# Performance work log

Hardware: AMD Instinct MI355X
Metric: run time of the kernel (lower is better)

Reference implementation:

```python
import jax, jax.numpy as jnp
import numpy as np

B, R, L, V, D, P, K = 512, 20, 50, 50000, 64, 2, 10
IN_DIM = 2 * P * D
TAU = 0.5


def _gating(x, w1, w2, b2, bg):
    # sigmoid(xW1^T) + bg * tanh(xW2^T + b2)
    return jax.nn.sigmoid(x @ w1.T) + bg * jnp.tanh(x @ w2.T + b2)


def _coatt_scores(u, i, w, b, M):
    uo = jax.nn.relu(u @ w.T + b)
    io = jax.nn.relu(i @ w.T + b)
    # bilinear scores: U @ M @ I^T
    return jnp.einsum('bud,de,bve->buv', uo, M, io)


def _gumbel_hard(logits, key):
    g = jax.random.gumbel(key, logits.shape, logits.dtype)
    y = jax.nn.softmax((logits + g) / TAU, axis=-1)
    yh = jax.nn.one_hot(jnp.argmax(y, axis=-1), logits.shape[-1], dtype=y.dtype)
    return y + jax.lax.stop_gradient(yh - y)  # straight-through hard one-hot


def _forward(user_reviews, item_reviews, emb, gate_w1, gate_w2, gate_b2, gate_bg,
             ra_w, ra_b, ra_M, wa_w, wa_b, wa_M, fm_v, fm_w, fm_b):
    u_emb = emb[user_reviews]            # [B,R,L,D]
    i_emb = emb[item_reviews]            # [B,R,L,D]
    u_rev = _gating(u_emb.sum(axis=-2), gate_w1, gate_w2, gate_b2, gate_bg)  # [B,R,D]
    i_rev = _gating(i_emb.sum(axis=-2), gate_w1, gate_w2, gate_b2, gate_bg)  # [B,R,D]
    key = jax.random.key(42)
    u_reprs, i_reprs = [], []
    for p in range(P):
        s = _coatt_scores(u_rev, i_rev, ra_w, ra_b, ra_M)     # [B,R,R]
        pr = _gumbel_hard(s.max(axis=-1), jax.random.fold_in(key, 2 * p))
        pc = _gumbel_hard(s.max(axis=-2), jax.random.fold_in(key, 2 * p + 1))
        # hard one-hot pointer 'gather' expressed as weighted sum over review axis
        ur = jnp.einsum('br,brld->bld', pr, u_emb)            # [B,L,D]
        ir = jnp.einsum('br,brld->bld', pc, i_emb)            # [B,L,D]
        sw = _coatt_scores(ur, ir, wa_w, wa_b, wa_M)          # [B,L,L]
        wr = jax.nn.softmax(sw.mean(axis=-1), axis=-1)        # [B,L]
        wc = jax.nn.softmax(sw.mean(axis=-2), axis=-1)        # [B,L]
        u_reprs.append(jnp.einsum('bl,bld->bd', wr, ur))
        i_reprs.append(jnp.einsum('bl,bld->bd', wc, ir))
    x = jnp.concatenate(u_reprs + i_reprs, axis=-1)           # [B, 2*P*D]
    lin = x @ fm_w.T + fm_b                                   # [B,1]
    i1 = x @ fm_v
    i2 = (x * x) @ (fm_v * fm_v)
    pair = jnp.sum(i1 * i1 - i2, axis=-1)                     # [B]
    return (lin[:, 0] + 0.5 * pair)[:, None]                  # [B,1]


def setup_inputs() -> dict:
    key = jax.random.key(0)
    ks = jax.random.split(key, 20)
    return {
        'user_reviews': jax.random.randint(ks[0], (B, R, L), 0, V, dtype=jnp.int32),
        'item_reviews': jax.random.randint(ks[1], (B, R, L), 0, V, dtype=jnp.int32),
        'emb': jax.random.normal(ks[2], (V, D), jnp.float32) * 0.1,
        'gate_w1': jax.random.normal(ks[3], (D, D), jnp.float32) * 0.05,
        'gate_w2': jax.random.normal(ks[4], (D, D), jnp.float32) * 0.05,
        'gate_b2': jax.random.normal(ks[5], (D,), jnp.float32) * 0.05,
        'gate_bg': jax.random.normal(ks[6], (D,), jnp.float32) * 0.05,
        'ra_w': jax.random.normal(ks[7], (D, D), jnp.float32) * 0.05,
        'ra_b': jax.random.normal(ks[8], (D,), jnp.float32) * 0.05,
        'ra_M': jax.random.normal(ks[9], (D, D), jnp.float32) * 0.05,
        'wa_w': jax.random.normal(ks[10], (D, D), jnp.float32) * 0.05,
        'wa_b': jax.random.normal(ks[11], (D,), jnp.float32) * 0.05,
        'wa_M': jax.random.normal(ks[12], (D, D), jnp.float32) * 0.05,
        'fm_v': jax.random.normal(ks[13], (IN_DIM, K), jnp.float32) * 0.05,
        'fm_w': jax.random.normal(ks[14], (1, IN_DIM), jnp.float32) * 0.05,
        'fm_b': jax.random.normal(ks[15], (1,), jnp.float32) * 0.05,
    }


def reference(user_reviews, item_reviews, emb, gate_w1, gate_w2, gate_b2, gate_bg,
              ra_w, ra_b, ra_M, wa_w, wa_b, wa_M, fm_v, fm_w, fm_b):
    return _forward(user_reviews, item_reviews, emb, gate_w1, gate_w2, gate_b2, gate_bg,
                    ra_w, ra_b, ra_M, wa_w, wa_b, wa_M, fm_v, fm_w, fm_b)
```

## Files before the change

kernel.cpp:

```cpp
#include <hip/hip_runtime.h>
#include <stdint.h>
#include <math.h>

#define BB 512
#define RR 20
#define LL 50
#define DD 64
#define PP 2
#define KK 10
#define IN_DIM 256
#define VV 50000
#define NEBLK 1280
#define NTBLK 782

__device__ __forceinline__ uint32_t rotl32(uint32_t v, int d) {
  return (v << d) | (v >> (32 - d));
}

__device__ __forceinline__ void tf2x32(uint32_t k0, uint32_t k1,
                                       uint32_t x0, uint32_t x1,
                                       uint32_t& o0, uint32_t& o1) {
  uint32_t ks0 = k0, ks1 = k1, ks2 = k0 ^ k1 ^ 0x1BD11BDAu;
  x0 += ks0; x1 += ks1;
#define TF_RND(r) { x0 += x1; x1 = rotl32(x1, r); x1 ^= x0; }
  TF_RND(13) TF_RND(15) TF_RND(26) TF_RND(6)
  x0 += ks1; x1 += ks2 + 1u;
  TF_RND(17) TF_RND(29) TF_RND(16) TF_RND(24)
  x0 += ks2; x1 += ks0 + 2u;
  TF_RND(13) TF_RND(15) TF_RND(26) TF_RND(6)
  x0 += ks0; x1 += ks1 + 3u;
  TF_RND(17) TF_RND(29) TF_RND(16) TF_RND(24)
  x0 += ks1; x1 += ks2 + 4u;
  TF_RND(13) TF_RND(15) TF_RND(26) TF_RND(6)
  x0 += ks2; x1 += ks0 + 5u;
#undef TF_RND
  o0 = x0; o1 = x1;
}

__device__ __forceinline__ float wave_sum(float v) {
  for (int off = 32; off; off >>= 1) v += __shfl_xor(v, off, 64);
  return v;
}
__device__ __forceinline__ float wave_max(float v) {
  for (int off = 32; off; off >>= 1) v = fmaxf(v, __shfl_xor(v, off, 64));
  return v;
}

__global__ __launch_bounds__(256) void transpose_w(
    const float* __restrict__ w1, const float* __restrict__ w2,
    const float* __restrict__ ra, const float* __restrict__ wa,
    const float* __restrict__ ma,
    float* __restrict__ w1T, float* __restrict__ w2T,
    float* __restrict__ raT, float* __restrict__ waT,
    float* __restrict__ maT) {
  int i = blockIdx.x * 256 + threadIdx.x;
  if (i < DD * DD) {
    int r = i >> 6, c = i & 63;
    w1T[c * DD + r] = w1[i];
    w2T[c * DD + r] = w2[i];
    raT[c * DD + r] = ra[i];
    waT[c * DD + r] = wa[i];
    maT[c * DD + r] = ma[i];
  }
}

__global__ __launch_bounds__(256, 4) void tables_embed(
    const int* __restrict__ uidx, const int* __restrict__ iidx,
    const float* __restrict__ emb,
    const float* __restrict__ w1T, const float* __restrict__ w2T,
    const float* __restrict__ b2, const float* __restrict__ bg,
    const float* __restrict__ waT, const float* __restrict__ wa_b,
    const float* __restrict__ maT,
    float* __restrict__ u_rev, float* __restrict__ i_rev,
    float* __restrict__ E1, float* __restrict__ E2) {
  __shared__ float smemA[DD * 68];
  __shared__ float smemB[DD * 68];
  int tid = threadIdx.x;
  int bid = blockIdx.x;

  if (bid < NEBLK) {
    int* idxs = (int*)smemA;
    float (*us)[68] = (float(*)[68])(smemA + 800);
    int isItem = (bid >= 640);
    const int* src = isItem ? (iidx + (size_t)(bid - 640) * 16 * LL)
                            : (uidx + (size_t)bid * 16 * LL);
    for (int i = tid; i < 16 * LL; i += 256) idxs[i] = src[i];
    __syncthreads();
    int w = tid >> 6, lane = tid & 63;
    int grp = lane >> 4, q = lane & 15;
    int revl = w * 4 + grp;
    const int* myidx = idxs + revl * LL;
    float4 acc = {0.f, 0.f, 0.f, 0.f};
#pragma unroll
    for (int l = 0; l < LL; ++l) {
      int v = myidx[l];
      float4 e4 = *reinterpret_cast<const float4*>(&emb[(size_t)v * DD + q * 4]);
      acc.x += e4.x; acc.y += e4.y; acc.z += e4.z; acc.w += e4.w;
    }
    *reinterpret_cast<float4*>(&us[revl][q * 4]) = acc;
    __syncthreads();
    float4 d1 = {0.f, 0.f, 0.f, 0.f}, d2 = {0.f, 0.f, 0.f, 0.f};
    for (int e = 0; e < DD; ++e) {
      float xv = us[revl][e];
      float4 w1v = *reinterpret_cast<const float4*>(&w1T[e * DD + q * 4]);
      float4 w2v = *reinterpret_cast<const float4*>(&w2T[e * DD + q * 4]);
      d1.x += xv * w1v.x; d1.y += xv * w1v.y; d1.z += xv * w1v.z; d1.w += xv * w1v.w;
      d2.x += xv * w2v.x; d2.y += xv * w2v.y; d2.z += xv * w2v.z; d2.w += xv * w2v.w;
    }
    float4 b2v = *reinterpret_cast<const float4*>(&b2[q * 4]);
    float4 bgv = *reinterpret_cast<const float4*>(&bg[q * 4]);
    float4 val;
    val.x = 1.f / (1.f + expf(-d1.x)) + bgv.x * tanhf(d2.x + b2v.x);
    val.y = 1.f / (1.f + expf(-d1.y)) + bgv.y * tanhf(d2.y + b2v.y);
    val.z = 1.f / (1.f + expf(-d1.z)) + bgv.z * tanhf(d2.z + b2v.z);
    val.w = 1.f / (1.f + expf(-d1.w)) + bgv.w * tanhf(d2.w + b2v.w);
    int gid = bid * 16 + revl;
    int t = gid - isItem * (BB * RR);
    float* dst = isItem ? i_rev : u_rev;
    *reinterpret_cast<float4*>(&dst[(size_t)t * DD + q * 4]) = val;
    return;
  }

  float* A  = smemA;
  float* Bs = smemB;
  int v0 = (bid - NEBLK) * 64;
  {
    int wr = tid & 63;
    int qk = tid >> 6;
    int v = v0 + wr;
    for (int rep = 0; rep < 4; ++rep) {
      int k0 = rep * 16 + qk * 4;
      float4 e4 = {0.f, 0.f, 0.f, 0.f};
      if (v < VV) e4 = *reinterpret_cast<const float4*>(&emb[(size_t)v * DD + k0]);
      A[(k0 + 0) * 68 + wr] = e4.x;
      A[(k0 + 1) * 68 + wr] = e4.y;
      A[(k0 + 2) * 68 + wr] = e4.z;
      A[(k0 + 3) * 68 + wr] = e4.w;
    }
  }
  for (int i = tid; i < DD * 16; i += 256) {
    int k = i >> 4, c = i & 15;
    *reinterpret_cast<float4*>(&Bs[k * 68 + c * 4]) =
        *reinterpret_cast<const float4*>(&waT[k * DD + c * 4]);
  }
  __syncthreads();
  int wq = tid & 15, dq = tid >> 4;
  float4 bias = *reinterpret_cast<const float4*>(&wa_b[dq * 4]);
  float acc[4][4];
#pragma unroll
  for (int i = 0; i < 4; ++i) {
    acc[i][0] = bias.x; acc[i][1] = bias.y; acc[i][2] = bias.z; acc[i][3] = bias.w;
  }
  for (int k = 0; k < DD; ++k) {
    float4 a4 = *reinterpret_cast<const float4*>(&A[k * 68 + wq * 4]);
    float4 b4 = *reinterpret_cast<const float4*>(&Bs[k * 68 + dq * 4]);
    float av[4] = {a4.x, a4.y, a4.z, a4.w};
    float bv[4] = {b4.x, b4.y, b4.z, b4.w};
#pragma unroll
    for (int i = 0; i < 4; ++i)
#pragma unroll
      for (int j = 0; j < 4; ++j) acc[i][j] += av[i] * bv[j];
  }
#pragma unroll
  for (int i = 0; i < 4; ++i)
#pragma unroll
    for (int j = 0; j < 4; ++j) acc[i][j] = fmaxf(acc[i][j], 0.f);
#pragma unroll
  for (int i = 0; i < 4; ++i) {
    int v = v0 + wq * 4 + i;
    if (v < VV) {
      float4 r = {acc[i][0], acc[i][1], acc[i][2], acc[i][3]};
      *reinterpret_cast<float4*>(&E1[(size_t)v * DD + dq * 4]) = r;
    }
  }
  __syncthreads();
#pragma unroll
  for (int j = 0; j < 4; ++j)
#pragma unroll
    for (int i = 0; i < 4; ++i)
      A[(dq * 4 + j) * 68 + wq * 4 + i] = acc[i][j];
  for (int i = tid; i < DD * 16; i += 256) {
    int k = i >> 4, c = i & 15;
    *reinterpret_cast<float4*>(&Bs[k * 68 + c * 4]) =
        *reinterpret_cast<const float4*>(&maT[k * DD + c * 4]);
  }
  __syncthreads();
  float acc2[4][4];
#pragma unroll
  for (int i = 0; i < 4; ++i)
#pragma unroll
    for (int j = 0; j < 4; ++j) acc2[i][j] = 0.f;
  for (int k = 0; k < DD; ++k) {
    float4 a4 = *reinterpret_cast<const float4*>(&A[k * 68 + wq * 4]);
    float4 b4 = *reinterpret_cast<const float4*>(&Bs[k * 68 + dq * 4]);
    float av[4] = {a4.x, a4.y, a4.z, a4.w};
    float bv[4] = {b4.x, b4.y, b4.z, b4.w};
#pragma unroll
    for (int i = 0; i < 4; ++i)
#pragma unroll
      for (int j = 0; j < 4; ++j) acc2[i][j] += av[i] * bv[j];
  }
#pragma unroll
  for (int i = 0; i < 4; ++i) {
    int v = v0 + wq * 4 + i;
    if (v < VV) {
      float4 r = {acc2[i][0], acc2[i][1], acc2[i][2], acc2[i][3]};
      *reinterpret_cast<float4*>(&E2[(size_t)v * DD + dq * 4]) = r;
    }
  }
}

__global__ __launch_bounds__(256) void coatt_rev_sel(
    const float* __restrict__ u_rev, const float* __restrict__ i_rev,
    const float* __restrict__ raT, const float* __restrict__ ra_b,
    const float* __restrict__ ra_M, int* __restrict__ sel) {
  int b = blockIdx.x;
  __shared__ float ur[RR * 68], ir[RR * 68], uo[RR * 68], io[RR * 68], au[RR * 68];
  __shared__ float sc[RR * 21];
  __shared__ float rl[RR], cl[RR];
  __shared__ float gval[4][RR];
  int tid = threadIdx.x;
  for (int i = tid; i < RR * 16; i += 256) {
    int r = i >> 4, qq = i & 15;
    *reinterpret_cast<float4*>(&ur[r * 68 + qq * 4]) =
        *reinterpret_cast<const float4*>(&u_rev[(size_t)b * RR * DD + r * DD + qq * 4]);
    *reinterpret_cast<float4*>(&ir[r * 68 + qq * 4]) =
        *reinterpret_cast<const float4*>(&i_rev[(size_t)b * RR * DD + r * DD + qq * 4]);
  }
  __syncthreads();
  for (int s = tid; s < RR * 16; s += 256) {
    int u = s >> 4, q = s & 15;
    float4 bias = *reinterpret_cast<const float4*>(&ra_b[q * 4]);
    float4 a1 = bias, a2 = bias;
    for (int e = 0; e < DD; ++e) {
      float xu = ur[u * 68 + e];
      float xi = ir[u * 68 + e];
      float4 wv = *reinterpret_cast<const float4*>(&raT[e * DD + q * 4]);
      a1.x += xu * wv.x; a1.y += xu * wv.y; a1.z += xu * wv.z; a1.w += xu * wv.w;
      a2.x += xi * wv.x; a2.y += xi * wv.y; a2.z += xi * wv.z; a2.w += xi * wv.w;
    }
    a1.x = fmaxf(a1.x, 0.f); a1.y = fmaxf(a1.y, 0.f);
    a1.z = fmaxf(a1.z, 0.f); a1.w = fmaxf(a1.w, 0.f);
    a2.x = fmaxf(a2.x, 0.f); a2.y = fmaxf(a2.y, 0.f);
    a2.z = fmaxf(a2.z, 0.f); a2.w = fmaxf(a2.w, 0.f);
    *reinterpret_cast<float4*>(&uo[u * 68 + q * 4]) = a1;
    *reinterpret_cast<float4*>(&io[u * 68 + q * 4]) = a2;
  }
  __syncthreads();
  for (int s = tid; s < RR * 16; s += 256) {
    int u = s >> 4, q = s & 15;
    float4 a = {0.f, 0.f, 0.f, 0.f};
    for (int d2 = 0; d2 < DD; ++d2) {
      float xv = uo[u * 68 + d2];
      float4 mv = *reinterpret_cast<const float4*>(&ra_M[d2 * DD + q * 4]);
      a.x += xv * mv.x; a.y += xv * mv.y; a.z += xv * mv.z; a.w += xv * mv.w;
    }
    *reinterpret_cast<float4*>(&au[u * 68 + q * 4]) = a;
  }
  __syncthreads();
  for (int i = tid; i < RR * RR; i += 256) {
    int u = i / RR, v = i % RR;
    float a = 0.f;
    for (int e = 0; e < DD; ++e) a += au[u * 68 + e] * io[v * 68 + e];
    sc[u * 21 + v] = a;
  }
  __syncthreads();
  if (tid < RR) {
    float m = -INFINITY;
    for (int v = 0; v < RR; ++v) m = fmaxf(m, sc[tid * 21 + v]);
    rl[tid] = m;
  } else if (tid >= 64 && tid < 64 + RR) {
    int v = tid - 64;
    float m = -INFINITY;
    for (int u = 0; u < RR; ++u) m = fmaxf(m, sc[u * 21 + v]);
    cl[v] = m;
  }
  __syncthreads();
  if (tid < 4 * RR) {
    int n = tid / RR, r = tid % RR;
    uint32_t k0, k1, o0, o1;
    tf2x32(0u, 42u, 0u, (uint32_t)n, k0, k1);
    int e = b * RR + r;
    tf2x32(k0, k1, 0u, (uint32_t)e, o0, o1);
    uint32_t bits = o0 ^ o1;
    float u01 = __uint_as_float((bits >> 9) | 0x3f800000u) - 1.0f;
    const float TINY = 1.1754943508222875e-38f;
    float u = fmaxf(u01 + TINY, TINY);
    float g = -logf(-logf(u));
    gval[n][r] = ((n & 1) ? cl[r] : rl[r]) + g;
  }
  __syncthreads();
  if (tid < 4) {
    float best = -INFINITY; int arg = 0;
    for (int r = 0; r < RR; ++r) {
      float v = gval[tid][r];
      if (v > best) { best = v; arg = r; }
    }
    sel[tid * BB + b] = arg;
  }
}

__global__ __launch_bounds__(256) void word_coatt(
    const int* __restrict__ uidx, const int* __restrict__ iidx,
    const float* __restrict__ emb,
    const float* __restrict__ E1, const float* __restrict__ E2,
    const int* __restrict__ sel, float* __restrict__ x) {
  int bid = blockIdx.x;
  int p = bid >> 9, b = bid & (BB - 1);
  int ru = sel[(2 * p) * BB + b];
  int rv = sel[(2 * p + 1) * BB + b];
  __shared__ int uw[LL], iw[LL];
  __shared__ float E1u[LL * 65], E2i[LL * 65];
  __shared__ float ubar[DD], zbar[DD];
  __shared__ float rm[LL], cm[LL];
  int tid = threadIdx.x;
  if (tid < LL) uw[tid] = uidx[((size_t)b * RR + ru) * LL + tid];
  else if (tid >= 64 && tid < 64 + LL) iw[tid - 64] = iidx[((size_t)b * RR + rv) * LL + (tid - 64)];
  __syncthreads();
  for (int i = tid; i < LL * DD; i += 256) {
    int l = i >> 6, d = i & 63;
    E1u[l * 65 + d] = E1[(size_t)uw[l] * DD + d];
    E2i[l * 65 + d] = E2[(size_t)iw[l] * DD + d];
  }
  __syncthreads();
  if (tid < DD) {
    float s = 0.f;
    for (int l = 0; l < LL; ++l) s += E1u[l * 65 + tid];
    ubar[tid] = s / 50.f;
  } else if (tid < 128) {
    int d = tid - 64;
    float s = 0.f;
    for (int l = 0; l < LL; ++l) s += E2i[l * 65 + d];
    zbar[d] = s / 50.f;
  }
  __syncthreads();
  if (tid < LL) {
    float a = 0.f;
    for (int e = 0; e < DD; ++e) a += E1u[tid * 65 + e] * zbar[e];
    rm[tid] = a;
  } else if (tid >= 64 && tid < 64 + LL) {
    int lj = tid - 64;
    float a = 0.f;
    for (int e = 0; e < DD; ++e) a += ubar[e] * E2i[lj * 65 + e];
    cm[lj] = a;
  }
  __syncthreads();
  int w = tid >> 6, lane = tid & 63;
  if (w == 0) {
    float v = (lane < LL) ? rm[lane] : -INFINITY;
    float m = wave_max(v);
    float ex = (lane < LL) ? expf(rm[lane] - m) : 0.f;
    float sm = wave_sum(ex);
    if (lane < LL) rm[lane] = ex / sm;
  } else if (w == 1) {
    float v = (lane < LL) ? cm[lane] : -INFINITY;
    float m = wave_max(v);
    float ex = (lane < LL) ? expf(cm[lane] - m) : 0.f;
    float sm = wave_sum(ex);
    if (lane < LL) cm[lane] = ex / sm;
  }
  __syncthreads();
  if (w == 0) {
    float a = 0.f;
    for (int l = 0; l < LL; ++l) a += rm[l] * emb[(size_t)uw[l] * DD + lane];
    x[(size_t)b * IN_DIM + p * DD + lane] = a;
  } else if (w == 1) {
    float a = 0.f;
    for (int l = 0; l < LL; ++l) a += cm[l] * emb[(size_t)iw[l] * DD + lane];
    x[(size_t)b * IN_DIM + 2 * DD + p * DD + lane] = a;
  }
}

__global__ __launch_bounds__(256) void fm_head(
    const float* __restrict__ x, const float* __restrict__ fm_v,
    const float* __restrict__ fm_w, const float* __restrict__ fm_b,
    float* __restrict__ out) {
  int tid = threadIdx.x;
  int w = tid >> 6, lane = tid & 63;
  int b = blockIdx.x * 4 + w;
  const float* xb = x + (size_t)b * IN_DIM;
  float4 xv4 = *reinterpret_cast<const float4*>(&xb[lane * 4]);
  float4 wv4 = *reinterpret_cast<const float4*>(&fm_w[lane * 4]);
  float xa[4] = {xv4.x, xv4.y, xv4.z, xv4.w};
  float wa[4] = {wv4.x, wv4.y, wv4.z, wv4.w};
  float lin = 0.f;
  float i1[KK], i2[KK];
#pragma unroll
  for (int k = 0; k < KK; ++k) { i1[k] = 0.f; i2[k] = 0.f; }
#pragma unroll
  for (int jj = 0; jj < 4; ++jj) {
    float xj = xa[jj];
    lin += xj * wa[jj];
    float x2 = xj * xj;
    const float* vr = fm_v + (size_t)(lane * 4 + jj) * KK;
#pragma unroll
    for (int k = 0; k < KK; ++k) {
      float v = vr[k];
      i1[k] += xj * v;
      i2[k] += x2 * (v * v);
    }
  }
  lin = wave_sum(lin);
  float pair = 0.f;
#pragma unroll
  for (int k = 0; k < KK; ++k) {
    float s1 = wave_sum(i1[k]);
    float s2 = wave_sum(i2[k]);
    pair += s1 * s1 - s2;
  }
  if (lane == 0) out[b] = (lin + fm_b[0]) + 0.5f * pair;
}

extern "C" void kernel_launch(void* const* d_in, const int* in_sizes, int n_in,
                              void* d_out, int out_size, void* d_ws, size_t ws_size,
                              hipStream_t stream) {
  (void)in_sizes; (void)n_in; (void)out_size; (void)ws_size;
  const int*   user_reviews = (const int*)d_in[0];
  const int*   item_reviews = (const int*)d_in[1];
  const float* emb  = (const float*)d_in[2];
  const float* gw1  = (const float*)d_in[3];
  const float* gw2  = (const float*)d_in[4];
  const float* gb2  = (const float*)d_in[5];
  const float* gbg  = (const float*)d_in[6];
  const float* ra_w = (const float*)d_in[7];
  const float* ra_b = (const float*)d_in[8];
  const float* ra_M = (const float*)d_in[9];
  const float* wa_w = (const float*)d_in[10];
  const float* wa_b = (const float*)d_in[11];
  const float* wa_M = (const float*)d_in[12];
  const float* fm_v = (const float*)d_in[13];
  const float* fm_w = (const float*)d_in[14];
  const float* fm_b = (const float*)d_in[15];
  float* out = (float*)d_out;

  float* ws = (float*)d_ws;
  float* u_rev = ws;
  float* i_rev = u_rev + BB * RR * DD;
  float* x     = i_rev + BB * RR * DD;
  float* w1T   = x + BB * IN_DIM;
  float* w2T   = w1T + DD * DD;
  float* raT   = w2T + DD * DD;
  float* waT   = raT + DD * DD;
  float* maT   = waT + DD * DD;
  float* E1    = maT + DD * DD;
  float* E2    = E1 + (size_t)VV * DD;
  int*   sel   = (int*)(E2 + (size_t)VV * DD);

  transpose_w<<<dim3(16), dim3(256), 0, stream>>>(gw1, gw2, ra_w, wa_w, wa_M,
                                                  w1T, w2T, raT, waT, maT);
  tables_embed<<<dim3(NEBLK + NTBLK), dim3(256), 0, stream>>>(
      user_reviews, item_reviews, emb, w1T, w2T, gb2, gbg,
      waT, wa_b, maT, u_rev, i_rev, E1, E2);
  coatt_rev_sel<<<dim3(BB), dim3(256), 0, stream>>>(
      u_rev, i_rev, raT, ra_b, ra_M, sel);
  word_coatt<<<dim3(PP * BB), dim3(256), 0, stream>>>(
      user_reviews, item_reviews, emb, E1, E2, sel, x);
  fm_head<<<dim3(128), dim3(256), 0, stream>>>(x, fm_v, fm_w, fm_b, out);
}
```

Before: 99.42 us.

## Fuse review coattention, word coattention and FM head into one kernel

Merges the review-selection, word-coattention and FM head kernels into a single per-batch-row kernel. Shared memory is reused across phases, and the selected indices and x vector stay on chip instead of going through global memory. This removes two launches and their global round trips. The word phase now loops over both pointers inside one block, so the grid drops from 1024 to 512 blocks. Separately, tables_embed stops staging the weight matrices in shared memory and reads them from global/cache, and drops the occupancy hint in its launch bounds.

```diff
diff --git a/kernel.cpp b/kernel.cpp
--- a/kernel.cpp
+++ b/kernel.cpp
@@ -64,7 +64,7 @@
   }
 }
 
-__global__ __launch_bounds__(256, 4) void tables_embed(
+__global__ __launch_bounds__(256) void tables_embed(
     const int* __restrict__ uidx, const int* __restrict__ iidx,
     const float* __restrict__ emb,
     const float* __restrict__ w1T, const float* __restrict__ w2T,
@@ -74,7 +74,6 @@
     float* __restrict__ u_rev, float* __restrict__ i_rev,
     float* __restrict__ E1, float* __restrict__ E2) {
   __shared__ float smemA[DD * 68];
-  __shared__ float smemB[DD * 68];
   int tid = threadIdx.x;
   int bid = blockIdx.x;
 
@@ -121,8 +120,7 @@
     return;
   }
 
-  float* A  = smemA;
-  float* Bs = smemB;
+  float* A = smemA;
   int v0 = (bid - NEBLK) * 64;
   {
     int wr = tid & 63;
@@ -138,11 +136,6 @@
       A[(k0 + 3) * 68 + wr] = e4.w;
     }
   }
-  for (int i = tid; i < DD * 16; i += 256) {
-    int k = i >> 4, c = i & 15;
-    *reinterpret_cast<float4*>(&Bs[k * 68 + c * 4]) =
-        *reinterpret_cast<const float4*>(&waT[k * DD + c * 4]);
-  }
   __syncthreads();
   int wq = tid & 15, dq = tid >> 4;
   float4 bias = *reinterpret_cast<const float4*>(&wa_b[dq * 4]);
@@ -153,7 +146,7 @@
   }
   for (int k = 0; k < DD; ++k) {
     float4 a4 = *reinterpret_cast<const float4*>(&A[k * 68 + wq * 4]);
-    float4 b4 = *reinterpret_cast<const float4*>(&Bs[k * 68 + dq * 4]);
+    float4 b4 = *reinterpret_cast<const float4*>(&waT[k * DD + dq * 4]);
     float av[4] = {a4.x, a4.y, a4.z, a4.w};
     float bv[4] = {b4.x, b4.y, b4.z, b4.w};
 #pragma unroll
@@ -179,11 +172,6 @@
 #pragma unroll
     for (int i = 0; i < 4; ++i)
       A[(dq * 4 + j) * 68 + wq * 4 + i] = acc[i][j];
-  for (int i = tid; i < DD * 16; i += 256) {
-    int k = i >> 4, c = i & 15;
-    *reinterpret_cast<float4*>(&Bs[k * 68 + c * 4]) =
-        *reinterpret_cast<const float4*>(&maT[k * DD + c * 4]);
-  }
   __syncthreads();
   float acc2[4][4];
 #pragma unroll
@@ -192,7 +180,7 @@
     for (int j = 0; j < 4; ++j) acc2[i][j] = 0.f;
   for (int k = 0; k < DD; ++k) {
     float4 a4 = *reinterpret_cast<const float4*>(&A[k * 68 + wq * 4]);
-    float4 b4 = *reinterpret_cast<const float4*>(&Bs[k * 68 + dq * 4]);
+    float4 b4 = *reinterpret_cast<const float4*>(&maT[k * DD + dq * 4]);
     float av[4] = {a4.x, a4.y, a4.z, a4.w};
     float bv[4] = {b4.x, b4.y, b4.z, b4.w};
 #pragma unroll
@@ -210,205 +198,212 @@
   }
 }
 
-__global__ __launch_bounds__(256) void coatt_rev_sel(
+__global__ __launch_bounds__(256) void coatt_word_fm(
     const float* __restrict__ u_rev, const float* __restrict__ i_rev,
     const float* __restrict__ raT, const float* __restrict__ ra_b,
-    const float* __restrict__ ra_M, int* __restrict__ sel) {
-  int b = blockIdx.x;
-  __shared__ float ur[RR * 68], ir[RR * 68], uo[RR * 68], io[RR * 68], au[RR * 68];
-  __shared__ float sc[RR * 21];
-  __shared__ float rl[RR], cl[RR];
-  __shared__ float gval[4][RR];
-  int tid = threadIdx.x;
-  for (int i = tid; i < RR * 16; i += 256) {
-    int r = i >> 4, qq = i & 15;
-    *reinterpret_cast<float4*>(&ur[r * 68 + qq * 4]) =
-        *reinterpret_cast<const float4*>(&u_rev[(size_t)b * RR * DD + r * DD + qq * 4]);
-    *reinterpret_cast<float4*>(&ir[r * 68 + qq * 4]) =
-        *reinterpret_cast<const float4*>(&i_rev[(size_t)b * RR * DD + r * DD + qq * 4]);
-  }
-  __syncthreads();
-  for (int s = tid; s < RR * 16; s += 256) {
-    int u = s >> 4, q = s & 15;
-    float4 bias = *reinterpret_cast<const float4*>(&ra_b[q * 4]);
-    float4 a1 = bias, a2 = bias;
-    for (int e = 0; e < DD; ++e) {
-      float xu = ur[u * 68 + e];
-      float xi = ir[u * 68 + e];
-      float4 wv = *reinterpret_cast<const float4*>(&raT[e * DD + q * 4]);
-      a1.x += xu * wv.x; a1.y += xu * wv.y; a1.z += xu * wv.z; a1.w += xu * wv.w;
-      a2.x += xi * wv.x; a2.y += xi * wv.y; a2.z += xi * wv.z; a2.w += xi * wv.w;
-    }
-    a1.x = fmaxf(a1.x, 0.f); a1.y = fmaxf(a1.y, 0.f);
-    a1.z = fmaxf(a1.z, 0.f); a1.w = fmaxf(a1.w, 0.f);
-    a2.x = fmaxf(a2.x, 0.f); a2.y = fmaxf(a2.y, 0.f);
-    a2.z = fmaxf(a2.z, 0.f); a2.w = fmaxf(a2.w, 0.f);
-    *reinterpret_cast<float4*>(&uo[u * 68 + q * 4]) = a1;
-    *reinterpret_cast<float4*>(&io[u * 68 + q * 4]) = a2;
-  }
-  __syncthreads();
-  for (int s = tid; s < RR * 16; s += 256) {
-    int u = s >> 4, q = s & 15;
-    float4 a = {0.f, 0.f, 0.f, 0.f};
-    for (int d2 = 0; d2 < DD; ++d2) {
-      float xv = uo[u * 68 + d2];
-      float4 mv = *reinterpret_cast<const float4*>(&ra_M[d2 * DD + q * 4]);
-      a.x += xv * mv.x; a.y += xv * mv.y; a.z += xv * mv.z; a.w += xv * mv.w;
-    }
-    *reinterpret_cast<float4*>(&au[u * 68 + q * 4]) = a;
-  }
-  __syncthreads();
-  for (int i = tid; i < RR * RR; i += 256) {
-    int u = i / RR, v = i % RR;
-    float a = 0.f;
-    for (int e = 0; e < DD; ++e) a += au[u * 68 + e] * io[v * 68 + e];
-    sc[u * 21 + v] = a;
-  }
-  __syncthreads();
-  if (tid < RR) {
-    float m = -INFINITY;
-    for (int v = 0; v < RR; ++v) m = fmaxf(m, sc[tid * 21 + v]);
-    rl[tid] = m;
-  } else if (tid >= 64 && tid < 64 + RR) {
-    int v = tid - 64;
-    float m = -INFINITY;
-    for (int u = 0; u < RR; ++u) m = fmaxf(m, sc[u * 21 + v]);
-    cl[v] = m;
-  }
-  __syncthreads();
-  if (tid < 4 * RR) {
-    int n = tid / RR, r = tid % RR;
-    uint32_t k0, k1, o0, o1;
-    tf2x32(0u, 42u, 0u, (uint32_t)n, k0, k1);
-    int e = b * RR + r;
-    tf2x32(k0, k1, 0u, (uint32_t)e, o0, o1);
-    uint32_t bits = o0 ^ o1;
-    float u01 = __uint_as_float((bits >> 9) | 0x3f800000u) - 1.0f;
-    const float TINY = 1.1754943508222875e-38f;
-    float u = fmaxf(u01 + TINY, TINY);
-    float g = -logf(-logf(u));
-    gval[n][r] = ((n & 1) ? cl[r] : rl[r]) + g;
-  }
-  __syncthreads();
-  if (tid < 4) {
-    float best = -INFINITY; int arg = 0;
-    for (int r = 0; r < RR; ++r) {
-      float v = gval[tid][r];
-      if (v > best) { best = v; arg = r; }
-    }
-    sel[tid * BB + b] = arg;
-  }
-}
-
-__global__ __launch_bounds__(256) void word_coatt(
+    const float* __restrict__ ra_M,
     const int* __restrict__ uidx, const int* __restrict__ iidx,
     const float* __restrict__ emb,
     const float* __restrict__ E1, const float* __restrict__ E2,
-    const int* __restrict__ sel, float* __restrict__ x) {
-  int bid = blockIdx.x;
-  int p = bid >> 9, b = bid & (BB - 1);
-  int ru = sel[(2 * p) * BB + b];
-  int rv = sel[(2 * p + 1) * BB + b];
-  __shared__ int uw[LL], iw[LL];
-  __shared__ float E1u[LL * 65], E2i[LL * 65];
-  __shared__ float ubar[DD], zbar[DD];
-  __shared__ float rm[LL], cm[LL];
+    const float* __restrict__ fm_v, const float* __restrict__ fm_w,
+    const float* __restrict__ fm_b, float* __restrict__ out) {
+  int b = blockIdx.x;
   int tid = threadIdx.x;
-  if (tid < LL) uw[tid] = uidx[((size_t)b * RR + ru) * LL + tid];
-  else if (tid >= 64 && tid < 64 + LL) iw[tid - 64] = iidx[((size_t)b * RR + rv) * LL + (tid - 64)];
+  __shared__ float smem[7340];
+  __shared__ float xb[IN_DIM];
+  __shared__ int sel4[4];
+
+  {
+    float* ur = smem;
+    float* ir = smem + 1360;
+    float* uo = smem + 2720;
+    float* io = smem + 4080;
+    float* au = smem + 5440;
+    float* sc = smem + 6800;
+    float* rl = smem + 7220;
+    float* cl = smem + 7240;
+    float (*gval)[RR] = (float(*)[RR])(smem + 7260);
+    for (int i = tid; i < RR * 16; i += 256) {
+      int r = i >> 4, qq = i & 15;
+      *reinterpret_cast<float4*>(&ur[r * 68 + qq * 4]) =
+          *reinterpret_cast<const float4*>(&u_rev[(size_t)b * RR * DD + r * DD + qq * 4]);
+      *reinterpret_cast<float4*>(&ir[r * 68 + qq * 4]) =
+          *reinterpret_cast<const float4*>(&i_rev[(size_t)b * RR * DD + r * DD + qq * 4]);
+    }
+    __syncthreads();
+    for (int s = tid; s < RR * 16; s += 256) {
+      int u = s >> 4, q = s & 15;
+      float4 bias = *reinterpret_cast<const float4*>(&ra_b[q * 4]);
+      float4 a1 = bias, a2 = bias;
+      for (int e = 0; e < DD; ++e) {
+        float xu = ur[u * 68 + e];
+        float xi = ir[u * 68 + e];
+        float4 wv = *reinterpret_cast<const float4*>(&raT[e * DD + q * 4]);
+        a1.x += xu * wv.x; a1.y += xu * wv.y; a1.z += xu * wv.z; a1.w += xu * wv.w;
+        a2.x += xi * wv.x; a2.y += xi * wv.y; a2.z += xi * wv.z; a2.w += xi * wv.w;
+      }
+      a1.x = fmaxf(a1.x, 0.f); a1.y = fmaxf(a1.y, 0.f);
+      a1.z = fmaxf(a1.z, 0.f); a1.w = fmaxf(a1.w, 0.f);
+      a2.x = fmaxf(a2.x, 0.f); a2.y = fmaxf(a2.y, 0.f);
+      a2.z = fmaxf(a2.z, 0.f); a2.w = fmaxf(a2.w, 0.f);
+      *reinterpret_cast<float4*>(&uo[u * 68 + q * 4]) = a1;
+      *reinterpret_cast<float4*>(&io[u * 68 + q * 4]) = a2;
+    }
+    __syncthreads();
+    for (int s = tid; s < RR * 16; s += 256) {
+      int u = s >> 4, q = s & 15;
+      float4 a = {0.f, 0.f, 0.f, 0.f};
+      for (int d2 = 0; d2 < DD; ++d2) {
+        float xv = uo[u * 68 + d2];
+        float4 mv = *reinterpret_cast<const float4*>(&ra_M[d2 * DD + q * 4]);
+        a.x += xv * mv.x; a.y += xv * mv.y; a.z += xv * mv.z; a.w += xv * mv.w;
+      }
+      *reinterpret_cast<float4*>(&au[u * 68 + q * 4]) = a;
+    }
+    __syncthreads();
+    for (int i = tid; i < RR * RR; i += 256) {
+      int u = i / RR, v = i % RR;
+      float a = 0.f;
+      for (int e = 0; e < DD; ++e) a += au[u * 68 + e] * io[v * 68 + e];
+      sc[u * 21 + v] = a;
+    }
+    __syncthreads();
+    if (tid < RR) {
+      float m = -INFINITY;
+      for (int v = 0; v < RR; ++v) m = fmaxf(m, sc[tid * 21 + v]);
+      rl[tid] = m;
+    } else if (tid >= 64 && tid < 64 + RR) {
+      int v = tid - 64;
+      float m = -INFINITY;
+      for (int u = 0; u < RR; ++u) m = fmaxf(m, sc[u * 21 + v]);
+      cl[v] = m;
+    }
+    __syncthreads();
+    if (tid < 4 * RR) {
+      int n = tid / RR, r = tid % RR;
+      uint32_t k0, k1, o0, o1;
+      tf2x32(0u, 42u, 0u, (uint32_t)n, k0, k1);
+      int e = b * RR + r;
+      tf2x32(k0, k1, 0u, (uint32_t)e, o0, o1);
+      uint32_t bits = o0 ^ o1;
+      float u01 = __uint_as_float((bits >> 9) | 0x3f800000u) - 1.0f;
+      const float TINY = 1.1754943508222875e-38f;
+      float u = fmaxf(u01 + TINY, TINY);
+      float g = -logf(-logf(u));
+      gval[n][r] = ((n & 1) ? cl[r] : rl[r]) + g;
+    }
+    __syncthreads();
+    if (tid < 4) {
+      float best = -INFINITY; int arg = 0;
+      for (int r = 0; r < RR; ++r) {
+        float v = gval[tid][r];
+        if (v > best) { best = v; arg = r; }
+      }
+      sel4[tid] = arg;
+    }
+  }
+
+  float* E1u = smem;
+  float* E2i = smem + 3250;
+  float* ubar = smem + 6500;
+  float* zbar = smem + 6564;
+  float* rm = smem + 6628;
+  float* cm = smem + 6678;
+  int* uw = (int*)(smem + 6728);
+  int* iw = (int*)(smem + 6778);
+  int w = tid >> 6, lane = tid & 63;
+  for (int p = 0; p < PP; ++p) {
+    __syncthreads();
+    int ru = sel4[2 * p], rv = sel4[2 * p + 1];
+    if (tid < LL) uw[tid] = uidx[((size_t)b * RR + ru) * LL + tid];
+    else if (tid >= 64 && tid < 64 + LL) iw[tid - 64] = iidx[((size_t)b * RR + rv) * LL + (tid - 64)];
+    __syncthreads();
+    for (int i = tid; i < LL * DD; i += 256) {
+      int l = i >> 6, d = i & 63;
+      E1u[l * 65 + d] = E1[(size_t)uw[l] * DD + d];
+      E2i[l * 65 + d] = E2[(size_t)iw[l] * DD + d];
+    }
+    __syncthreads();
+    if (tid < DD) {
+      float s = 0.f;
+      for (int l = 0; l < LL; ++l) s += E1u[l * 65 + tid];
+      ubar[tid] = s / 50.f;
+    } else if (tid < 128) {
+      int d = tid - 64;
+      float s = 0.f;
+      for (int l = 0; l < LL; ++l) s += E2i[l * 65 + d];
+      zbar[d] = s / 50.f;
+    }
+    __syncthreads();
+    if (tid < LL) {
+      float a = 0.f;
+      for (int e = 0; e < DD; ++e) a += E1u[tid * 65 + e] * zbar[e];
+      rm[tid] = a;
+    } else if (tid >= 64 && tid < 64 + LL) {
+      int lj = tid - 64;
+      float a = 0.f;
+      for (int e = 0; e < DD; ++e) a += ubar[e] * E2i[lj * 65 + e];
+      cm[lj] = a;
+    }
+    __syncthreads();
+    if (w == 0) {
+      float v = (lane < LL) ? rm[lane] : -INFINITY;
+      float m = wave_max(v);
+      float ex = (lane < LL) ? expf(rm[lane] - m) : 0.f;
+      float sm = wave_sum(ex);
+      if (lane < LL) rm[lane] = ex / sm;
+    } else if (w == 1) {
+      float v = (lane < LL) ? cm[lane] : -INFINITY;
+      float m = wave_max(v);
+      float ex = (lane < LL) ? expf(cm[lane] - m) : 0.f;
+      float sm = wave_sum(ex);
+      if (lane < LL) cm[lane] = ex / sm;
+    }
+    __syncthreads();
+    if (w == 0) {
+      float a = 0.f;
+      for (int l = 0; l < LL; ++l) a += rm[l] * emb[(size_t)uw[l] * DD + lane];
+      xb[p * DD + lane] = a;
+    } else if (w == 1) {
+      float a = 0.f;
+      for (int l = 0; l < LL; ++l) a += cm[l] * emb[(size_t)iw[l] * DD + lane];
+      xb[2 * DD + p * DD + lane] = a;
+    }
+  }
   __syncthreads();
-  for (int i = tid; i < LL * DD; i += 256) {
-    int l = i >> 6, d = i & 63;
-    E1u[l * 65 + d] = E1[(size_t)uw[l] * DD + d];
-    E2i[l * 65 + d] = E2[(size_t)iw[l] * DD + d];
-  }
-  __syncthreads();
-  if (tid < DD) {
-    float s = 0.f;
-    for (int l = 0; l < LL; ++l) s += E1u[l * 65 + tid];
-    ubar[tid] = s / 50.f;
-  } else if (tid < 128) {
-    int d = tid - 64;
-    float s = 0.f;
-    for (int l = 0; l < LL; ++l) s += E2i[l * 65 + d];
-    zbar[d] = s / 50.f;
-  }
-  __syncthreads();
-  if (tid < LL) {
-    float a = 0.f;
-    for (int e = 0; e < DD; ++e) a += E1u[tid * 65 + e] * zbar[e];
-    rm[tid] = a;
-  } else if (tid >= 64 && tid < 64 + LL) {
-    int lj = tid - 64;
-    float a = 0.f;
-    for (int e = 0; e < DD; ++e) a += ubar[e] * E2i[lj * 65 + e];
-    cm[lj] = a;
-  }
-  __syncthreads();
-  int w = tid >> 6, lane = tid & 63;
-  if (w == 0) {
-    float v = (lane < LL) ? rm[lane] : -INFINITY;
-    float m = wave_max(v);
-    float ex = (lane < LL) ? expf(rm[lane] - m) : 0.f;
-    float sm = wave_sum(ex);
-    if (lane < LL) rm[lane] = ex / sm;
-  } else if (w == 1) {
-    float v = (lane < LL) ? cm[lane] : -INFINITY;
-    float m = wave_max(v);
-    float ex = (lane < LL) ? expf(cm[lane] - m) : 0.f;
-    float sm = wave_sum(ex);
-    if (lane < LL) cm[lane] = ex / sm;
-  }
-  __syncthreads();
-  if (w == 0) {
-    float a = 0.f;
-    for (int l = 0; l < LL; ++l) a += rm[l] * emb[(size_t)uw[l] * DD + lane];
-    x[(size_t)b * IN_DIM + p * DD + lane] = a;
-  } else if (w == 1) {
-    float a = 0.f;
-    for (int l = 0; l < LL; ++l) a += cm[l] * emb[(size_t)iw[l] * DD + lane];
-    x[(size_t)b * IN_DIM + 2 * DD + p * DD + lane] = a;
-  }
-}
-
-__global__ __launch_bounds__(256) void fm_head(
-    const float* __restrict__ x, const float* __restrict__ fm_v,
-    const float* __restrict__ fm_w, const float* __restrict__ fm_b,
-    float* __restrict__ out) {
-  int tid = threadIdx.x;
-  int w = tid >> 6, lane = tid & 63;
-  int b = blockIdx.x * 4 + w;
-  const float* xb = x + (size_t)b * IN_DIM;
-  float4 xv4 = *reinterpret_cast<const float4*>(&xb[lane * 4]);
-  float4 wv4 = *reinterpret_cast<const float4*>(&fm_w[lane * 4]);
-  float xa[4] = {xv4.x, xv4.y, xv4.z, xv4.w};
-  float wa[4] = {wv4.x, wv4.y, wv4.z, wv4.w};
-  float lin = 0.f;
-  float i1[KK], i2[KK];
-#pragma unroll
-  for (int k = 0; k < KK; ++k) { i1[k] = 0.f; i2[k] = 0.f; }
-#pragma unroll
-  for (int jj = 0; jj < 4; ++jj) {
-    float xj = xa[jj];
-    lin += xj * wa[jj];
-    float x2 = xj * xj;
-    const float* vr = fm_v + (size_t)(lane * 4 + jj) * KK;
+
+  if (tid < 64) {
+    float4 xv4 = *reinterpret_cast<const float4*>(&xb[tid * 4]);
+    float4 wv4 = *reinterpret_cast<const float4*>(&fm_w[tid * 4]);
+    float xa[4] = {xv4.x, xv4.y, xv4.z, xv4.w};
+    float wa[4] = {wv4.x, wv4.y, wv4.z, wv4.w};
+    float lin = 0.f;
+    float i1[KK], i2[KK];
+#pragma unroll
+    for (int k = 0; k < KK; ++k) { i1[k] = 0.f; i2[k] = 0.f; }
+#pragma unroll
+    for (int jj = 0; jj < 4; ++jj) {
+      float xj = xa[jj];
+      lin += xj * wa[jj];
+      float x2 = xj * xj;
+      const float* vr = fm_v + (size_t)(tid * 4 + jj) * KK;
+#pragma unroll
+      for (int k = 0; k < KK; ++k) {
+        float v = vr[k];
+        i1[k] += xj * v;
+        i2[k] += x2 * (v * v);
+      }
+    }
+    lin = wave_sum(lin);
+    float pair = 0.f;
 #pragma unroll
     for (int k = 0; k < KK; ++k) {
-      float v = vr[k];
-      i1[k] += xj * v;
-      i2[k] += x2 * (v * v);
-    }
-  }
-  lin = wave_sum(lin);
-  float pair = 0.f;
-#pragma unroll
-  for (int k = 0; k < KK; ++k) {
-    float s1 = wave_sum(i1[k]);
-    float s2 = wave_sum(i2[k]);
-    pair += s1 * s1 - s2;
-  }
-  if (lane == 0) out[b] = (lin + fm_b[0]) + 0.5f * pair;
+      float s1 = wave_sum(i1[k]);
+      float s2 = wave_sum(i2[k]);
+      pair += s1 * s1 - s2;
+    }
+    if (tid == 0) out[b] = (lin + fm_b[0]) + 0.5f * pair;
+  }
 }
 
 extern "C" void kernel_launch(void* const* d_in, const int* in_sizes, int n_in,
@@ -436,24 +431,21 @@
   float* ws = (float*)d_ws;
   float* u_rev = ws;
   float* i_rev = u_rev + BB * RR * DD;
-  float* x     = i_rev + BB * RR * DD;
-  float* w1T   = x + BB * IN_DIM;
+  float* w1T   = i_rev + BB * RR * DD;
   float* w2T   = w1T + DD * DD;
   float* raT   = w2T + DD * DD;
   float* waT   = raT + DD * DD;
   float* maT   = waT + DD * DD;
   float* E1    = maT + DD * DD;
   float* E2    = E1 + (size_t)VV * DD;
-  int*   sel   = (int*)(E2 + (size_t)VV * DD);
 
   transpose_w<<<dim3(16), dim3(256), 0, stream>>>(gw1, gw2, ra_w, wa_w, wa_M,
                                                   w1T, w2T, raT, waT, maT);
   tables_embed<<<dim3(NEBLK + NTBLK), dim3(256), 0, stream>>>(
       user_reviews, item_reviews, emb, w1T, w2T, gb2, gbg,
       waT, wa_b, maT, u_rev, i_rev, E1, E2);
-  coatt_rev_sel<<<dim3(BB), dim3(256), 0, stream>>>(
-      u_rev, i_rev, raT, ra_b, ra_M, sel);
-  word_coatt<<<dim3(PP * BB), dim3(256), 0, stream>>>(
-      user_reviews, item_reviews, emb, E1, E2, sel, x);
-  fm_head<<<dim3(128), dim3(256), 0, stream>>>(x, fm_v, fm_w, fm_b, out);
-}
+  coatt_word_fm<<<dim3(BB), dim3(256), 0, stream>>>(
+      u_rev, i_rev, raT, ra_b, ra_M,
+      user_reviews, item_reviews, emb, E1, E2,
+      fm_v, fm_w, fm_b, out);
+}
```

After: 123.9 us. +24.6%, slower.
